# Kernel tuning notes

Hardware: AMD Instinct MI355X
Metric: run time of the kernel (lower is better)

Reference implementation:

```python
import jax, jax.numpy as jnp
import numpy as np

GAMMA = 2.0
CONTEXT_WINDOW = 100


def setup_inputs() -> dict:
    key = jax.random.key(0)
    k1, k2 = jax.random.split(key)
    B, S, C = 64, 131072, 3
    inputs = jax.random.normal(k1, (B, S, C), dtype=jnp.float32)
    targets = jax.random.randint(k2, (B, S), 0, C, dtype=jnp.int32)
    alpha = jnp.array([0.25, 1.0, 1.0], dtype=jnp.float32)
    return {"inputs": inputs, "targets": targets, "alpha": alpha}


def _window_mask(targets, window):
    # mask[b, i] = True iff any positive target within +/- window of i;
    # rows with no positives are fully True (matches torch loop semantics).
    B, S = targets.shape
    pos = targets > 0                                   # (B, S) bool
    cs = jnp.cumsum(pos.astype(jnp.int32), axis=1)      # inclusive prefix sums
    c = jnp.concatenate([jnp.zeros((B, 1), jnp.int32), cs], axis=1)  # (B, S+1)
    idx = jnp.arange(S)
    hi = jnp.minimum(idx + window + 1, S)               # exclusive end
    lo = jnp.maximum(idx - window, 0)                   # inclusive start
    count = c[:, hi] - c[:, lo]                         # positives in window
    mask = count > 0
    has_pos = pos.any(axis=1, keepdims=True)
    return jnp.where(has_pos, mask, True)


def reference(inputs, targets, alpha):
    # inputs: (B, S, C) logits; targets: (B, S) class indices
    mask = _window_mask(targets, CONTEXT_WINDOW)                     # (B, S)
    logp = jax.nn.log_softmax(inputs, axis=-1)                       # (B, S, C)
    ce = -jnp.take_along_axis(logp, targets[..., None].astype(jnp.int32), axis=-1)[..., 0]
    p_t = jnp.exp(-ce)
    focal = alpha[targets] * (1.0 - p_t) ** GAMMA * ce               # (B, S)
    m = mask.astype(inputs.dtype)
    # masked mean == mean over selected elements in the torch version
    return jnp.sum(focal * m) / jnp.sum(m)
```

## Files before the change

kernel.cpp:

```cpp
#include <hip/hip_runtime.h>

#define BB 64
#define SS 131072
#define WIN 100
#define TILE 4096
#define NTHREADS 256
#define TILES_PER_ROW (SS / TILE)
#define NBLOCKS (BB * TILES_PER_ROW)
#define EXT (TILE + 2*WIN)
#define NWORDS ((EXT + 63) / 64)
#define SH_BYTES (NWORDS * 64)
#define K4TOT (SH_BYTES / 4)
#define SROUNDS ((K4TOT + NTHREADS - 1) / NTHREADS)
#define NGROUPS 4
#define GF4 (NTHREADS * 3)

typedef float  fx4 __attribute__((ext_vector_type(4)));
typedef int    ix4 __attribute__((ext_vector_type(4)));

__global__ __launch_bounds__(NTHREADS, 5) void focal_main(
    const float* __restrict__ inputs, const int* __restrict__ targets,
    const float* __restrict__ alpha, double* __restrict__ slots)
{
    __shared__ __align__(16) unsigned char sh_t[SH_BYTES];
    __shared__ unsigned long long wbits[NWORDS];
    __shared__ unsigned long long mbits[NWORDS];
    __shared__ fx4 buf[2][GF4];
    __shared__ double red[(NTHREADS/64) * 4];

    const int t = threadIdx.x;
    const int b = blockIdx.x / TILES_PER_ROW;
    const int tile = blockIdx.x % TILES_PER_ROW;
    const int s0 = tile * TILE;
    const int ext_lo = (s0 - WIN > 0) ? (s0 - WIN) : 0;
    const int ext_hi = (s0 + TILE + WIN < SS) ? (s0 + TILE + WIN) : SS;
    const int ext_len = ext_hi - ext_lo;
    const int tr_lo = s0 - ext_lo;

    const float* inrow = inputs + (long)b * SS * 3;
    const fx4* gbase = (const fx4*)(inrow + (long)s0 * 3);
    fx4 q0 = __builtin_nontemporal_load(gbase + t);
    fx4 q1 = __builtin_nontemporal_load(gbase + NTHREADS + t);
    fx4 q2 = __builtin_nontemporal_load(gbase + 2 * NTHREADS + t);

    const int* trow = targets + (long)b * SS;
    #pragma unroll
    for (int it = 0; it < SROUNDS; ++it) {
        const int k4 = it * NTHREADS + t;
        if (k4 < K4TOT) {
            unsigned int pk = 0;
            if (4 * k4 < ext_len) {
                const ix4 tv4 =
                    __builtin_nontemporal_load((const ix4*)(trow + ext_lo + 4 * k4));
                pk = (unsigned)(tv4.x & 3) | ((unsigned)(tv4.y & 3) << 8) |
                     ((unsigned)(tv4.z & 3) << 16) | ((unsigned)(tv4.w & 3) << 24);
            }
            ((unsigned int*)sh_t)[k4] = pk;
        }
    }
    __syncthreads();

    int cnt_p = 0;
    if (t < NWORDS) {
        const uint4* qp = (const uint4*)(sh_t + (t << 6));
        unsigned long long wv = 0;
        #pragma unroll
        for (int r = 0; r < 4; ++r) {
            const uint4 u = qp[r];
            unsigned int x, nz;
            x = u.x; nz = (x | (x >> 1)) & 0x01010101u;
            wv |= (unsigned long long)((nz * 0x01020408u) >> 24) << (r*16 + 0);
            x = u.y; nz = (x | (x >> 1)) & 0x01010101u;
            wv |= (unsigned long long)((nz * 0x01020408u) >> 24) << (r*16 + 4);
            x = u.z; nz = (x | (x >> 1)) & 0x01010101u;
            wv |= (unsigned long long)((nz * 0x01020408u) >> 24) << (r*16 + 8);
            x = u.w; nz = (x | (x >> 1)) & 0x01010101u;
            wv |= (unsigned long long)((nz * 0x01020408u) >> 24) << (r*16 + 12);
        }
        wbits[t] = wv;
        int lo_bit = tr_lo - (t << 6);        if (lo_bit < 0) lo_bit = 0;
        int hi_bit = tr_lo + TILE - (t << 6); if (hi_bit > 64) hi_bit = 64;
        if (hi_bit > lo_bit) {
            unsigned long long rm = (hi_bit >= 64) ? ~0ULL : ((1ULL << hi_bit) - 1);
            rm &= (~0ULL << lo_bit);
            cnt_p = __popcll(wv & rm);
        }
    }
    __syncthreads();

    if (t < NWORDS) {
        const unsigned long long a = (t >= 2) ? wbits[t-2] : 0ULL;
        const unsigned long long bw = (t >= 1) ? wbits[t-1] : 0ULL;
        const unsigned long long c = wbits[t];
        const unsigned long long d = (t+1 < NWORDS) ? wbits[t+1] : 0ULL;
        const unsigned long long e = (t+2 < NWORDS) ? wbits[t+2] : 0ULL;
        unsigned long long m = c ? ~0ULL : 0ULL;
        if (d) { const int lo = __builtin_ctzll(d) - 36;
                 m |= (lo <= 0) ? ~0ULL : (~0ULL << lo); }
        if (e) { const int lo = __builtin_ctzll(e) + 28;
                 if (lo <= 63) m |= (~0ULL << lo); }
        if (bw) { const int hi = 63 - __builtin_clzll(bw) + 36;
                  m |= (hi >= 63) ? ~0ULL : (~0ULL >> (63 - hi)); }
        if (a) { const int hi = 63 - __builtin_clzll(a) - 28;
                 if (hi >= 0) m |= (hi >= 63) ? ~0ULL : (~0ULL >> (63 - hi)); }
        mbits[t] = m;
    }
    __syncthreads();

    buf[0][t] = q0; buf[0][NTHREADS + t] = q1; buf[0][2*NTHREADS + t] = q2;
    {
        const fx4* g1src = (const fx4*)(inrow + (long)(s0 + 1024) * 3);
        q0 = __builtin_nontemporal_load(g1src + t);
        q1 = __builtin_nontemporal_load(g1src + NTHREADS + t);
        q2 = __builtin_nontemporal_load(g1src + 2 * NTHREADS + t);
    }
    __syncthreads();

    const float a0 = alpha[0], a1 = alpha[1], a2 = alpha[2];
    float fsum_m = 0.0f, fsum_a = 0.0f;
    int cnt_m = 0;

    #pragma unroll
    for (int g = 0; g < NGROUPS; ++g) {
        const fx4* my = (const fx4*)((const float*)buf[g & 1] + t * 12);
        const fx4 c0 = my[0], c1 = my[1], c2 = my[2];

        if (g + 1 < NGROUPS) {
            buf[(g+1) & 1][t] = q0;
            buf[(g+1) & 1][NTHREADS + t] = q1;
            buf[(g+1) & 1][2*NTHREADS + t] = q2;
        }
        if (g + 2 < NGROUPS) {
            const fx4* gn = (const fx4*)(inrow + (long)(s0 + (g+2) * 1024) * 3);
            q0 = __builtin_nontemporal_load(gn + t);
            q1 = __builtin_nontemporal_load(gn + NTHREADS + t);
            q2 = __builtin_nontemporal_load(gn + 2 * NTHREADS + t);
        }

        const int p = s0 + g * 1024 + t * 4;
        const int j0 = p - ext_lo;
        const unsigned long long mw = mbits[j0 >> 6];
        const unsigned int tpack = *(const unsigned int*)(sh_t + j0);
        const float xs[12] = {c0.x, c0.y, c0.z, c0.w, c1.x, c1.y, c1.z, c1.w,
                              c2.x, c2.y, c2.z, c2.w};
        #pragma unroll
        for (int j = 0; j < 4; ++j) {
            const float x0 = xs[3*j], x1 = xs[3*j+1], x2 = xs[3*j+2];
            const int tv = (tpack >> (8 * j)) & 0xFF;
            const float mx = fmaxf(x0, fmaxf(x1, x2));
            const float mn = fminf(x0, fminf(x1, x2));
            const float md = fmaxf(fminf(x0, x1), fminf(fmaxf(x0, x1), x2));
            const float emd = __expf(md - mx);
            const float emn = __expf(mn - mx);
            const float sum = 1.0f + emd + emn;
            const float xt  = (tv == 0) ? x0 : ((tv == 1) ? x1 : x2);
            const float et  = (xt == mx) ? 1.0f : ((xt == md) ? emd : emn);
            const float ce  = __logf(sum) + (mx - xt);
            const float pt  = et * __frcp_rn(sum);
            const float w   = (tv == 0) ? a0 : ((tv == 1) ? a1 : a2);
            const float om  = 1.0f - pt;
            const float focal = w * om * om * ce;
            const bool  m   = (mw >> ((j0 & 63) + j)) & 1ULL;

            fsum_a += focal;
            fsum_m += m ? focal : 0.0f;
            cnt_m  += m ? 1 : 0;
        }
        if (g + 1 < NGROUPS) __syncthreads();
    }

    const int wave = t >> 6, lane = t & 63;
    #pragma unroll
    for (int off = 32; off >= 1; off >>= 1) {
        fsum_m += __shfl_down(fsum_m, off);
        fsum_a += __shfl_down(fsum_a, off);
        cnt_m  += __shfl_down(cnt_m, off);
        cnt_p  += __shfl_down(cnt_p, off);
    }
    if (lane == 0) {
        red[wave*4]   = (double)fsum_m; red[wave*4+1] = (double)cnt_m;
        red[wave*4+2] = (double)fsum_a; red[wave*4+3] = (double)cnt_p;
    }
    __syncthreads();
    if (t == 0) {
        double sm = 0, sc = 0, sa = 0, sp = 0;
        #pragma unroll
        for (int w = 0; w < NTHREADS/64; ++w) {
            sm += red[w*4]; sc += red[w*4+1]; sa += red[w*4+2]; sp += red[w*4+3];
        }
        double* slot = slots + (long)blockIdx.x * 4;
        slot[0] = sm;
        slot[1] = sc;
        slot[2] = sa;
        slot[3] = sp;
    }
}

__global__ __launch_bounds__(NTHREADS) void focal_final(
    const double* __restrict__ slots, float* __restrict__ out)
{
    __shared__ double red[(NTHREADS/64) * 2];
    __shared__ double tot[2];
    const int t = threadIdx.x;
    const int wave = t >> 6, lane = t & 63;

    double sm = 0.0, sc = 0.0;
    for (int k = t; k < NBLOCKS; k += NTHREADS) {
        sm += slots[(long)k * 4 + 0];
        sc += slots[(long)k * 4 + 1];
    }
    #pragma unroll
    for (int off = 32; off >= 1; off >>= 1) {
        sm += __shfl_down(sm, off);
        sc += __shfl_down(sc, off);
    }
    if (lane == 0) { red[wave*2] = sm; red[wave*2+1] = sc; }
    __syncthreads();
    if (t == 0) {
        double a = 0, b = 0;
        #pragma unroll
        for (int w = 0; w < NTHREADS/64; ++w) { a += red[w*2]; b += red[w*2+1]; }
        tot[0] = a; tot[1] = b;
    }
    __syncthreads();

    double corr_s = 0.0, corr_c = 0.0;
    if (t < BB) {
        double row_sum = 0.0, row_pos = 0.0;
        for (int j = 0; j < TILES_PER_ROW; ++j) {
            const long blk = (long)t * TILES_PER_ROW + j;
            row_sum += slots[blk * 4 + 2];
            row_pos += slots[blk * 4 + 3];
        }
        if (row_pos == 0.0) { corr_s = row_sum; corr_c = (double)SS; }
    }
    if (wave == 0) {
        #pragma unroll
        for (int off = 32; off >= 1; off >>= 1) {
            corr_s += __shfl_down(corr_s, off);
            corr_c += __shfl_down(corr_c, off);
        }
        if (t == 0) {
            const double total = tot[0] + corr_s;
            const double count = tot[1] + corr_c;
            out[0] = (float)(total / count);
        }
    }
}

extern "C" void kernel_launch(void* const* d_in, const int* in_sizes, int n_in,
                              void* d_out, int out_size, void* d_ws, size_t ws_size,
                              hipStream_t stream) {
    const float* inputs  = (const float*)d_in[0];
    const int*   targets = (const int*)d_in[1];
    const float* alpha   = (const float*)d_in[2];
    float* out = (float*)d_out;

    double* slots = (double*)d_ws;

    focal_main<<<NBLOCKS, NTHREADS, 0, stream>>>(inputs, targets, alpha, slots);
    focal_final<<<1, NTHREADS, 0, stream>>>(slots, out);
}
```

Baseline: 170.1 us.

## Load all logits into registers up front and parallelize final reduction

Drops the LDS double-buffer staging of logits. Each thread now issues all twelve 16-byte loads of its contiguous 12-float chunks at kernel start, then computes directly from registers without intermediate syncthreads. The final reduction kernel moves to 1024 threads, with per-row correction sums done by 16-lane shuffles instead of a serial 32-iteration loop per thread. This raises register pressure, which may reduce occupancy, and per-thread strided 48-byte access may coalesce less well than the old lane-contiguous loads.

```diff
diff --git a/kernel.cpp b/kernel.cpp
--- a/kernel.cpp
+++ b/kernel.cpp
@@ -13,10 +13,42 @@
 #define K4TOT (SH_BYTES / 4)
 #define SROUNDS ((K4TOT + NTHREADS - 1) / NTHREADS)
 #define NGROUPS 4
-#define GF4 (NTHREADS * 3)
 
 typedef float  fx4 __attribute__((ext_vector_type(4)));
 typedef int    ix4 __attribute__((ext_vector_type(4)));
+
+__device__ __forceinline__ void process4(
+    const fx4 c0, const fx4 c1, const fx4 c2,
+    const int j0, const unsigned long long mw, const unsigned int tpack,
+    const float a0, const float a1, const float a2,
+    float& fsum_m, float& fsum_a, int& cnt_m)
+{
+    const float xs[12] = {c0.x, c0.y, c0.z, c0.w, c1.x, c1.y, c1.z, c1.w,
+                          c2.x, c2.y, c2.z, c2.w};
+    #pragma unroll
+    for (int j = 0; j < 4; ++j) {
+        const float x0 = xs[3*j], x1 = xs[3*j+1], x2 = xs[3*j+2];
+        const int tv = (tpack >> (8 * j)) & 0xFF;
+        const float mx = fmaxf(x0, fmaxf(x1, x2));
+        const float mn = fminf(x0, fminf(x1, x2));
+        const float md = fmaxf(fminf(x0, x1), fminf(fmaxf(x0, x1), x2));
+        const float emd = __expf(md - mx);
+        const float emn = __expf(mn - mx);
+        const float sum = 1.0f + emd + emn;
+        const float xt  = (tv == 0) ? x0 : ((tv == 1) ? x1 : x2);
+        const float et  = (xt == mx) ? 1.0f : ((xt == md) ? emd : emn);
+        const float ce  = __logf(sum) + (mx - xt);
+        const float pt  = et * __frcp_rn(sum);
+        const float w   = (tv == 0) ? a0 : ((tv == 1) ? a1 : a2);
+        const float om  = 1.0f - pt;
+        const float focal = w * om * om * ce;
+        const bool  m   = (mw >> ((j0 & 63) + j)) & 1ULL;
+
+        fsum_a += focal;
+        fsum_m += m ? focal : 0.0f;
+        cnt_m  += m ? 1 : 0;
+    }
+}
 
 __global__ __launch_bounds__(NTHREADS, 5) void focal_main(
     const float* __restrict__ inputs, const int* __restrict__ targets,
@@ -25,7 +57,6 @@
     __shared__ __align__(16) unsigned char sh_t[SH_BYTES];
     __shared__ unsigned long long wbits[NWORDS];
     __shared__ unsigned long long mbits[NWORDS];
-    __shared__ fx4 buf[2][GF4];
     __shared__ double red[(NTHREADS/64) * 4];
 
     const int t = threadIdx.x;
@@ -39,9 +70,24 @@
 
     const float* inrow = inputs + (long)b * SS * 3;
     const fx4* gbase = (const fx4*)(inrow + (long)s0 * 3);
-    fx4 q0 = __builtin_nontemporal_load(gbase + t);
-    fx4 q1 = __builtin_nontemporal_load(gbase + NTHREADS + t);
-    fx4 q2 = __builtin_nontemporal_load(gbase + 2 * NTHREADS + t);
+    const fx4* p0 = gbase + t * 3;
+    const fx4* p1 = gbase + 768 + t * 3;
+    const fx4* p2 = gbase + 1536 + t * 3;
+    const fx4* p3 = gbase + 2304 + t * 3;
+    const fx4 q0  = __builtin_nontemporal_load(p0 + 0);
+    const fx4 q1  = __builtin_nontemporal_load(p0 + 1);
+    const fx4 q2  = __builtin_nontemporal_load(p0 + 2);
+    const fx4 q3  = __builtin_nontemporal_load(p1 + 0);
+    const fx4 q4  = __builtin_nontemporal_load(p1 + 1);
+    const fx4 q5  = __builtin_nontemporal_load(p1 + 2);
+    const fx4 q6  = __builtin_nontemporal_load(p2 + 0);
+    const fx4 q7  = __builtin_nontemporal_load(p2 + 1);
+    const fx4 q8  = __builtin_nontemporal_load(p2 + 2);
+    const fx4 q9  = __builtin_nontemporal_load(p3 + 0);
+    const fx4 q10 = __builtin_nontemporal_load(p3 + 1);
+    const fx4 q11 = __builtin_nontemporal_load(p3 + 2);
+
+    const float a0 = alpha[0], a1 = alpha[1], a2 = alpha[2];
 
     const int* trow = targets + (long)b * SS;
     #pragma unroll
@@ -107,66 +153,25 @@
     }
     __syncthreads();
 
-    buf[0][t] = q0; buf[0][NTHREADS + t] = q1; buf[0][2*NTHREADS + t] = q2;
-    {
-        const fx4* g1src = (const fx4*)(inrow + (long)(s0 + 1024) * 3);
-        q0 = __builtin_nontemporal_load(g1src + t);
-        q1 = __builtin_nontemporal_load(g1src + NTHREADS + t);
-        q2 = __builtin_nontemporal_load(g1src + 2 * NTHREADS + t);
-    }
-    __syncthreads();
-
-    const float a0 = alpha[0], a1 = alpha[1], a2 = alpha[2];
     float fsum_m = 0.0f, fsum_a = 0.0f;
     int cnt_m = 0;
-
-    #pragma unroll
-    for (int g = 0; g < NGROUPS; ++g) {
-        const fx4* my = (const fx4*)((const float*)buf[g & 1] + t * 12);
-        const fx4 c0 = my[0], c1 = my[1], c2 = my[2];
-
-        if (g + 1 < NGROUPS) {
-            buf[(g+1) & 1][t] = q0;
-            buf[(g+1) & 1][NTHREADS + t] = q1;
-            buf[(g+1) & 1][2*NTHREADS + t] = q2;
-        }
-        if (g + 2 < NGROUPS) {
-            const fx4* gn = (const fx4*)(inrow + (long)(s0 + (g+2) * 1024) * 3);
-            q0 = __builtin_nontemporal_load(gn + t);
-            q1 = __builtin_nontemporal_load(gn + NTHREADS + t);
-            q2 = __builtin_nontemporal_load(gn + 2 * NTHREADS + t);
-        }
-
-        const int p = s0 + g * 1024 + t * 4;
-        const int j0 = p - ext_lo;
-        const unsigned long long mw = mbits[j0 >> 6];
-        const unsigned int tpack = *(const unsigned int*)(sh_t + j0);
-        const float xs[12] = {c0.x, c0.y, c0.z, c0.w, c1.x, c1.y, c1.z, c1.w,
-                              c2.x, c2.y, c2.z, c2.w};
-        #pragma unroll
-        for (int j = 0; j < 4; ++j) {
-            const float x0 = xs[3*j], x1 = xs[3*j+1], x2 = xs[3*j+2];
-            const int tv = (tpack >> (8 * j)) & 0xFF;
-            const float mx = fmaxf(x0, fmaxf(x1, x2));
-            const float mn = fminf(x0, fminf(x1, x2));
-            const float md = fmaxf(fminf(x0, x1), fminf(fmaxf(x0, x1), x2));
-            const float emd = __expf(md - mx);
-            const float emn = __expf(mn - mx);
-            const float sum = 1.0f + emd + emn;
-            const float xt  = (tv == 0) ? x0 : ((tv == 1) ? x1 : x2);
-            const float et  = (xt == mx) ? 1.0f : ((xt == md) ? emd : emn);
-            const float ce  = __logf(sum) + (mx - xt);
-            const float pt  = et * __frcp_rn(sum);
-            const float w   = (tv == 0) ? a0 : ((tv == 1) ? a1 : a2);
-            const float om  = 1.0f - pt;
-            const float focal = w * om * om * ce;
-            const bool  m   = (mw >> ((j0 & 63) + j)) & 1ULL;
-
-            fsum_a += focal;
-            fsum_m += m ? focal : 0.0f;
-            cnt_m  += m ? 1 : 0;
-        }
-        if (g + 1 < NGROUPS) __syncthreads();
+    {
+        int j0 = tr_lo + t * 4;
+        process4(q0, q1, q2, j0, mbits[j0 >> 6],
+                 *(const unsigned int*)(sh_t + j0),
+                 a0, a1, a2, fsum_m, fsum_a, cnt_m);
+        j0 += 1024;
+        process4(q3, q4, q5, j0, mbits[j0 >> 6],
+                 *(const unsigned int*)(sh_t + j0),
+                 a0, a1, a2, fsum_m, fsum_a, cnt_m);
+        j0 += 1024;
+        process4(q6, q7, q8, j0, mbits[j0 >> 6],
+                 *(const unsigned int*)(sh_t + j0),
+                 a0, a1, a2, fsum_m, fsum_a, cnt_m);
+        j0 += 1024;
+        process4(q9, q10, q11, j0, mbits[j0 >> 6],
+                 *(const unsigned int*)(sh_t + j0),
+                 a0, a1, a2, fsum_m, fsum_a, cnt_m);
     }
 
     const int wave = t >> 6, lane = t & 63;
@@ -196,16 +201,17 @@
     }
 }
 
-__global__ __launch_bounds__(NTHREADS) void focal_final(
+__global__ __launch_bounds__(1024) void focal_final(
     const double* __restrict__ slots, float* __restrict__ out)
 {
-    __shared__ double red[(NTHREADS/64) * 2];
-    __shared__ double tot[2];
+    __shared__ double redA[16 * 2];
+    __shared__ double crs[BB];
+    __shared__ double crc[BB];
     const int t = threadIdx.x;
     const int wave = t >> 6, lane = t & 63;
 
     double sm = 0.0, sc = 0.0;
-    for (int k = t; k < NBLOCKS; k += NTHREADS) {
+    for (int k = t; k < NBLOCKS; k += 1024) {
         sm += slots[(long)k * 4 + 0];
         sc += slots[(long)k * 4 + 1];
     }
@@ -214,37 +220,31 @@
         sm += __shfl_down(sm, off);
         sc += __shfl_down(sc, off);
     }
-    if (lane == 0) { red[wave*2] = sm; red[wave*2+1] = sc; }
-    __syncthreads();
+    if (lane == 0) { redA[wave*2] = sm; redA[wave*2+1] = sc; }
+
+    const int row = t >> 4;
+    const int rpart = t & 15;
+    const long base = (long)row * TILES_PER_ROW + rpart * 2;
+    double rs = slots[base*4 + 2] + slots[(base+1)*4 + 2];
+    double rp = slots[base*4 + 3] + slots[(base+1)*4 + 3];
+    #pragma unroll
+    for (int off = 8; off >= 1; off >>= 1) {
+        rs += __shfl_down(rs, off, 16);
+        rp += __shfl_down(rp, off, 16);
+    }
+    if (rpart == 0) { crs[row] = rs; crc[row] = rp; }
+    __syncthreads();
+
     if (t == 0) {
-        double a = 0, b = 0;
-        #pragma unroll
-        for (int w = 0; w < NTHREADS/64; ++w) { a += red[w*2]; b += red[w*2+1]; }
-        tot[0] = a; tot[1] = b;
-    }
-    __syncthreads();
-
-    double corr_s = 0.0, corr_c = 0.0;
-    if (t < BB) {
-        double row_sum = 0.0, row_pos = 0.0;
-        for (int j = 0; j < TILES_PER_ROW; ++j) {
-            const long blk = (long)t * TILES_PER_ROW + j;
-            row_sum += slots[blk * 4 + 2];
-            row_pos += slots[blk * 4 + 3];
-        }
-        if (row_pos == 0.0) { corr_s = row_sum; corr_c = (double)SS; }
-    }
-    if (wave == 0) {
-        #pragma unroll
-        for (int off = 32; off >= 1; off >>= 1) {
-            corr_s += __shfl_down(corr_s, off);
-            corr_c += __shfl_down(corr_c, off);
-        }
-        if (t == 0) {
-            const double total = tot[0] + corr_s;
-            const double count = tot[1] + corr_c;
-            out[0] = (float)(total / count);
-        }
+        double a = 0.0, bsum = 0.0;
+        #pragma unroll
+        for (int w = 0; w < 16; ++w) { a += redA[w*2]; bsum += redA[w*2+1]; }
+        double corr_s = 0.0, corr_c = 0.0;
+        #pragma unroll
+        for (int r = 0; r < BB; ++r) {
+            if (crc[r] == 0.0) { corr_s += crs[r]; corr_c += (double)SS; }
+        }
+        out[0] = (float)((a + corr_s) / (bsum + corr_c));
     }
 }
 
@@ -259,5 +259,5 @@
     double* slots = (double*)d_ws;
 
     focal_main<<<NBLOCKS, NTHREADS, 0, stream>>>(inputs, targets, alpha, slots);
-    focal_final<<<1, NTHREADS, 0, stream>>>(slots, out);
-}
+    focal_final<<<1, 1024, 0, stream>>>(slots, out);
+}
```

New measurement: 178.1 us. +4.7%, slower.
